# Kernel optimization log

Hardware: AMD Instinct MI355X
Metric: run time of the kernel (lower is better)

The kernel has to match this reference:

```python
import jax, jax.numpy as jnp
import numpy as np

D = 1024      # model_size
H = 16        # n_heads
HD = D // H   # head_size
B = 8
S = 1024


def setup_inputs() -> dict:
    key = jax.random.key(0)
    ks = jax.random.split(key, 8)
    sq = lambda k, shp: jax.random.normal(k, shp, dtype=jnp.float32) * (1.0 / np.sqrt(shp[0]))
    return {
        "query": jax.random.normal(ks[0], (B, S, D), dtype=jnp.float32),
        "value": jax.random.normal(ks[1], (B, S, D), dtype=jnp.float32),
        "Wq": sq(ks[2], (D, D)),
        "bq": jnp.zeros((D,), dtype=jnp.float32),
        "Wkv": sq(ks[3], (D, 2 * D)),
        "bkv": jnp.zeros((2 * D,), dtype=jnp.float32),
        "Wo": sq(ks[4], (D, D)),
        "bo": jnp.zeros((D,), dtype=jnp.float32),
    }


def reference(query, value, Wq, bq, Wkv, bkv, Wo, bo):
    scale = 1.0 / jnp.sqrt(jnp.float32(HD))
    q = query @ Wq + bq                      # [B,S,D]
    kv = value @ Wkv + bkv                   # [B,S,2D]
    # tf.split(kv, 2H): chunks 0..H-1 are K heads, H..2H-1 are V heads
    k = kv[..., :D].reshape(B, S, H, HD)
    v = kv[..., D:].reshape(B, S, H, HD)
    qh = q.reshape(B, S, H, HD)
    scores = jnp.einsum("bqhd,bkhd->bhqk", qh, k) * scale   # [B,H,S,S]
    attn = jax.nn.softmax(scores, axis=-1)
    heads = jnp.einsum("bhqk,bkhd->bqhd", attn, v).reshape(B, S, D)
    return heads @ Wo + bo
```

## Files before the change

### kernel.cpp

```cpp
#include <hip/hip_runtime.h>
#include <math.h>

#define B_  8
#define S_  1024
#define D_  1024
#define H_  16
#define HD_ 64

typedef float          floatx4  __attribute__((ext_vector_type(4)));
typedef __bf16         bf16x8   __attribute__((ext_vector_type(8)));
typedef unsigned short ushortx4 __attribute__((ext_vector_type(4)));
typedef unsigned int   uintx2   __attribute__((ext_vector_type(2)));
typedef unsigned int   uintx4   __attribute__((ext_vector_type(4)));

__device__ __forceinline__ unsigned short f2bf(float f) {
    union { float f; unsigned u; } v; v.f = f;
    unsigned r = v.u + 0x7FFFu + ((v.u >> 16) & 1u);
    return (unsigned short)(r >> 16);
}
__device__ __forceinline__ unsigned pk2(float a, float b) {
    union { __bf16 h[2]; unsigned u; } r;
    r.h[0] = (__bf16)a; r.h[1] = (__bf16)b;
    return r.u;
}
__device__ __forceinline__ void async16(const void* g, void* l) {
    __builtin_amdgcn_global_load_lds(
        (__attribute__((address_space(1))) void*)g,
        (__attribute__((address_space(3))) void*)l, 16, 0, 0);
}

__global__ __launch_bounds__(256) void cast2_k(const float* __restrict__ s0,
                                               const float* __restrict__ s1,
                                               unsigned short* __restrict__ d0,
                                               unsigned short* __restrict__ d1) {
    int i = blockIdx.x * 256 + threadIdx.x;
    floatx4 a = ((const floatx4*)s0)[i];
    floatx4 b = ((const floatx4*)s1)[i];
    ushortx4 oa = { f2bf(a[0]), f2bf(a[1]), f2bf(a[2]), f2bf(a[3]) };
    ushortx4 ob = { f2bf(b[0]), f2bf(b[1]), f2bf(b[2]), f2bf(b[3]) };
    ((ushortx4*)d0)[i] = oa;
    ((ushortx4*)d1)[i] = ob;
}

__global__ __launch_bounds__(256) void wtrans_all_k(const float* __restrict__ Wq,
                                                    const float* __restrict__ Wkv,
                                                    const float* __restrict__ Wo,
                                                    unsigned short* __restrict__ WqT,
                                                    unsigned short* __restrict__ WkvT,
                                                    unsigned short* __restrict__ WoT) {
    __shared__ float T[64 * 68];
    const int t = threadIdx.x;
    const int z = blockIdx.z;
    const float* W; unsigned short* WT; int Ndim, nbase;
    if (z == 0)      { W = Wq;  WT = WqT;  Ndim = 1024; nbase = 0; }
    else if (z == 3) { W = Wo;  WT = WoT;  Ndim = 1024; nbase = 0; }
    else             { W = Wkv; WT = WkvT; Ndim = 2048; nbase = (z - 1) * 1024; }
    const int n0 = blockIdx.x * 64 + nbase;
    const int k0 = blockIdx.y * 64;
#pragma unroll
    for (int rep = 0; rep < 4; ++rep) {
        int kl = (t >> 4) + rep * 16;
        int ns = (t & 15) * 4;
        *(floatx4*)(T + kl * 68 + ns) = *(const floatx4*)(W + (size_t)(k0 + kl) * Ndim + n0 + ns);
    }
    __syncthreads();
#pragma unroll
    for (int rep = 0; rep < 2; ++rep) {
        int nl = (t >> 3) + rep * 32;
        int ks = (t & 7) * 8;
        union { unsigned short s[8]; uintx4 u; } o;
#pragma unroll
        for (int j = 0; j < 8; ++j) o.s[j] = f2bf(T[(ks + j) * 68 + nl]);
        *(uintx4*)(WT + (size_t)(n0 + nl) * 1024 + k0 + ks) = o.u;
    }
}

__global__ __launch_bounds__(256) void vtrans_k(const unsigned short* __restrict__ KVb,
                                                unsigned short* __restrict__ Vtg) {
    __shared__ unsigned short T[64 * 72];
    const int t  = threadIdx.x;
    const int c0 = blockIdx.x * 64;
    const int s0 = blockIdx.y * 64;
    const int b  = blockIdx.z;
#pragma unroll
    for (int rep = 0; rep < 2; ++rep) {
        int sl = (t >> 3) + rep * 32;
        int cs = (t & 7) * 8;
        *(uintx4*)(T + sl * 72 + cs) =
            *(const uintx4*)(KVb + ((size_t)(b * 1024 + s0 + sl)) * 2048 + 1024 + c0 + cs);
    }
    __syncthreads();
#pragma unroll
    for (int rep = 0; rep < 2; ++rep) {
        int cl = (t >> 3) + rep * 32;
        int ss = (t & 7) * 8;
        union { unsigned short s[8]; uintx4 u; } o;
#pragma unroll
        for (int j = 0; j < 8; ++j) o.s[j] = T[(ss + j) * 72 + cl];
        *(uintx4*)(Vtg + ((size_t)(b * 1024 + c0 + cl)) * 1024 + s0 + ss) = o.u;
    }
}

template<int OUT_BF16>
__global__ __launch_bounds__(256) void gemm_bt(const unsigned short* __restrict__ A,
                                               const unsigned short* __restrict__ Bt,
                                               const float* __restrict__ bias,
                                               void* __restrict__ C,
                                               int M, int N, int K, float oscale) {
    __shared__ unsigned short As[128 * 32];
    __shared__ unsigned short Bs[128 * 32];
    const int t    = threadIdx.x;
    const int lane = t & 63;
    const int w    = t >> 6;
    const int quad = lane >> 4;
    const int l15  = lane & 15;
    const int m0   = blockIdx.x * 128;
    const int n0   = blockIdx.y * 128;
    const int wr   = (w >> 1) * 64;
    const int wc   = (w & 1) * 64;
    const int rowA = lane >> 2;
    const int kseg = (lane & 3) * 8;

    floatx4 acc[4][4] = {};

    const unsigned short* ga0 = A  + (size_t)(m0 + rowA) * K + kseg;
    const unsigned short* gb0 = Bt + (size_t)(n0 + rowA) * K + kseg;

    for (int k0 = 0; k0 < K; k0 += 32) {
#pragma unroll
        for (int i = 0; i < 2; ++i) {
            int c = i * 4 + w;
            async16(ga0 + (size_t)(c * 16) * K + k0, As + c * 512);
            async16(gb0 + (size_t)(c * 16) * K + k0, Bs + c * 512);
        }
        __syncthreads();
        bf16x8 af[4], bf[4];
#pragma unroll
        for (int mi = 0; mi < 4; ++mi)
            af[mi] = *(const bf16x8*)(As + (wr + mi * 16 + l15) * 32 + quad * 8);
#pragma unroll
        for (int ni = 0; ni < 4; ++ni)
            bf[ni] = *(const bf16x8*)(Bs + (wc + ni * 16 + l15) * 32 + quad * 8);
#pragma unroll
        for (int mi = 0; mi < 4; ++mi)
#pragma unroll
            for (int ni = 0; ni < 4; ++ni)
                acc[mi][ni] = __builtin_amdgcn_mfma_f32_16x16x32_bf16(af[mi], bf[ni], acc[mi][ni], 0, 0, 0);
        __syncthreads();
    }

#pragma unroll
    for (int ni = 0; ni < 4; ++ni) {
        const int col = n0 + wc + ni * 16 + l15;
        const float bv = bias[col];
#pragma unroll
        for (int mi = 0; mi < 4; ++mi) {
            const int row = m0 + wr + mi * 16 + quad * 4;
#pragma unroll
            for (int r = 0; r < 4; ++r) {
                float v = (acc[mi][ni][r] + bv) * oscale;
                if (OUT_BF16)
                    ((unsigned short*)C)[(size_t)(row + r) * N + col] = f2bf(v);
                else
                    ((float*)C)[(size_t)(row + r) * N + col] = v;
            }
        }
    }
}

__global__ __launch_bounds__(256) void attn_kernel(const unsigned short* __restrict__ Qb,
                                                   const unsigned short* __restrict__ KVb,
                                                   const unsigned short* __restrict__ Vtg,
                                                   unsigned short* __restrict__ Hb) {
    __shared__ unsigned short Qs[128 * 64];
    __shared__ unsigned short Ks[64 * 64];
    __shared__ unsigned short Vs[64 * 64];
    __shared__ unsigned short Ps[4 * 32 * 64];

    const int lin = blockIdx.x;
    const int xcd = lin & 7;
    const int grp = lin >> 3;
    const int bh  = xcd * 16 + (grp >> 3);
    const int qt  = grp & 7;
    const int b   = bh >> 4;
    const int h   = bh & 15;
    const int q0  = qt * 128;

    const int t    = threadIdx.x;
    const int lane = t & 63;
    const int w    = t >> 6;
    const int quad = lane >> 4;
    const int l15  = lane & 15;
    const int e7   = l15 & 7;
    const int lrow = lane >> 3;
    const int lswz = ((lane & 7) ^ lrow) * 8;

    {
        const unsigned short* gq = Qb + ((size_t)(b * S_ + q0)) * D_ + h * HD_;
#pragma unroll
        for (int i = 0; i < 4; ++i) {
            int r0 = (w * 4 + i) * 8;
            async16(gq + (size_t)(r0 + lrow) * D_ + lswz, Qs + r0 * 64);
        }
    }

    const unsigned short* gkbase = KVb + ((size_t)b * S_) * (2 * D_) + h * HD_;
    const unsigned short* gvbase = Vtg + ((size_t)(b * D_ + h * HD_)) * S_;

    float   lsum[2] = { 0.f, 0.f };
    floatx4 oacc[4][2] = {};
    unsigned short* Psw = Ps + w * (32 * 64);

    for (int k0 = 0; k0 < S_; k0 += 64) {
        __syncthreads();
#pragma unroll
        for (int j = 0; j < 2; ++j) {
            int r0 = (w * 2 + j) * 8;
            async16(gkbase + (size_t)(k0 + r0 + lrow) * (2 * D_) + lswz, Ks + r0 * 64);
            async16(gvbase + (size_t)(r0 + lrow) * S_ + k0 + lswz,      Vs + r0 * 64);
        }
        __syncthreads();

        floatx4 st[4][2] = {};
#pragma unroll
        for (int ks = 0; ks < 2; ++ks) {
            bf16x8 aK[4], bQ[2];
#pragma unroll
            for (int mi = 0; mi < 4; ++mi)
                aK[mi] = *(const bf16x8*)(Ks + (mi * 16 + l15) * 64 + ((ks * 4 + quad) ^ e7) * 8);
#pragma unroll
            for (int ni = 0; ni < 2; ++ni)
                bQ[ni] = *(const bf16x8*)(Qs + (w * 32 + ni * 16 + l15) * 64 + ((ks * 4 + quad) ^ e7) * 8);
#pragma unroll
            for (int mi = 0; mi < 4; ++mi)
#pragma unroll
                for (int ni = 0; ni < 2; ++ni)
                    st[mi][ni] = __builtin_amdgcn_mfma_f32_16x16x32_bf16(aK[mi], bQ[ni], st[mi][ni], 0, 0, 0);
        }

#pragma unroll
        for (int ni = 0; ni < 2; ++ni) {
            float ls = 0.f;
#pragma unroll
            for (int mi = 0; mi < 4; ++mi) {
                float p0 = __builtin_amdgcn_exp2f(st[mi][ni][0]);
                float p1 = __builtin_amdgcn_exp2f(st[mi][ni][1]);
                float p2 = __builtin_amdgcn_exp2f(st[mi][ni][2]);
                float p3 = __builtin_amdgcn_exp2f(st[mi][ni][3]);
                ls += (p0 + p1) + (p2 + p3);
                uintx2 pk = { pk2(p0, p1), pk2(p2, p3) };
                *(uintx2*)(Psw + (ni * 16 + l15) * 64 +
                           (((2 * mi + (quad >> 1)) ^ e7) * 8 + (quad & 1) * 4)) = pk;
            }
            lsum[ni] += ls;
        }

#pragma unroll
        for (int ks = 0; ks < 2; ++ks) {
            bf16x8 aV[4], bP[2];
#pragma unroll
            for (int mi = 0; mi < 4; ++mi)
                aV[mi] = *(const bf16x8*)(Vs + (mi * 16 + l15) * 64 + ((ks * 4 + quad) ^ e7) * 8);
#pragma unroll
            for (int ni = 0; ni < 2; ++ni)
                bP[ni] = *(const bf16x8*)(Psw + (ni * 16 + l15) * 64 + ((ks * 4 + quad) ^ e7) * 8);
#pragma unroll
            for (int mi = 0; mi < 4; ++mi)
#pragma unroll
                for (int ni = 0; ni < 2; ++ni)
                    oacc[mi][ni] = __builtin_amdgcn_mfma_f32_16x16x32_bf16(aV[mi], bP[ni], oacc[mi][ni], 0, 0, 0);
        }
    }

    float rl[2];
#pragma unroll
    for (int ni = 0; ni < 2; ++ni) {
        float l = lsum[ni];
        l += __shfl_xor(l, 16);
        l += __shfl_xor(l, 32);
        rl[ni] = 1.f / l;
    }
#pragma unroll
    for (int mi = 0; mi < 4; ++mi)
#pragma unroll
        for (int ni = 0; ni < 2; ++ni) {
            uintx2 pk = { pk2(oacc[mi][ni][0] * rl[ni], oacc[mi][ni][1] * rl[ni]),
                          pk2(oacc[mi][ni][2] * rl[ni], oacc[mi][ni][3] * rl[ni]) };
            *(uintx2*)(Psw + (ni * 16 + l15) * 64 +
                       (((2 * mi + (quad >> 1)) ^ e7) * 8 + (quad & 1) * 4)) = pk;
        }
    {
        int qrow = lane >> 1;
        int kh   = lane & 1;
        size_t obase = ((size_t)(b * S_ + q0 + w * 32 + qrow)) * D_ + h * HD_ + kh * 32;
        int e = qrow & 7;
#pragma unroll
        for (int j = 0; j < 4; ++j) {
            int chunk = kh * 4 + j;
            *(uintx4*)(Hb + obase + j * 8) =
                *(const uintx4*)(Psw + qrow * 64 + ((chunk ^ e) * 8));
        }
    }
}

extern "C" void kernel_launch(void* const* d_in, const int* in_sizes, int n_in,
                              void* d_out, int out_size, void* d_ws, size_t ws_size,
                              hipStream_t stream) {
    (void)in_sizes; (void)n_in; (void)out_size; (void)ws_size;
    const float* query = (const float*)d_in[0];
    const float* value = (const float*)d_in[1];
    const float* Wq    = (const float*)d_in[2];
    const float* bq    = (const float*)d_in[3];
    const float* Wkv   = (const float*)d_in[4];
    const float* bkv   = (const float*)d_in[5];
    const float* Wo    = (const float*)d_in[6];
    const float* bo    = (const float*)d_in[7];

    const size_t MS = (size_t)B_ * S_;
    char* p = (char*)d_ws;
    unsigned short* qbf  = (unsigned short*)p; p += MS * D_ * 2;
    unsigned short* vbf  = (unsigned short*)p; p += MS * D_ * 2;
    unsigned short* WqT  = (unsigned short*)p; p += (size_t)D_ * D_ * 2;
    unsigned short* WkvT = (unsigned short*)p; p += (size_t)2 * D_ * D_ * 2;
    unsigned short* WoT  = (unsigned short*)p; p += (size_t)D_ * D_ * 2;
    unsigned short* Qb   = (unsigned short*)p; p += MS * D_ * 2;
    unsigned short* KVb  = (unsigned short*)p; p += MS * 2 * D_ * 2;
    unsigned short* Hb   = (unsigned short*)p; p += MS * D_ * 2;
    unsigned short* Vtg  = qbf;

    const float cexp = 0.125f * 1.44269504088896341f;

    cast2_k<<<(int)(MS * D_ / 1024), 256, 0, stream>>>(query, value, qbf, vbf);
    wtrans_all_k<<<dim3(16, 16, 4), 256, 0, stream>>>(Wq, Wkv, Wo, WqT, WkvT, WoT);

    gemm_bt<1><<<dim3(64, 8),  256, 0, stream>>>(qbf, WqT,  bq,  Qb,  8192, 1024, 1024, cexp);
    gemm_bt<1><<<dim3(64, 16), 256, 0, stream>>>(vbf, WkvT, bkv, KVb, 8192, 2048, 1024, 1.0f);
    vtrans_k<<<dim3(16, 16, 8), 256, 0, stream>>>(KVb, Vtg);
    attn_kernel<<<1024, 256, 0, stream>>>(Qb, KVb, Vtg, Hb);
    gemm_bt<0><<<dim3(64, 8),  256, 0, stream>>>(Hb, WoT, bo, d_out, 8192, 1024, 1024, 1.0f);
}
```

Before: 313.2 us.

## Fuse prep kernels, write V transposed from KV GEMM, hoist Q fragments

Merges the input cast and weight transpose into one launch, and drops the separate V-transpose kernel by having the KV GEMM's V half write its output directly in transposed layout. The K output becomes a compact [M,1024] buffer. The GEMM epilogue swaps MFMA operand order so it can issue vectorized stores, and the attention kernel keeps Q fragments in registers so its Q shared buffer can be reused for P. Together these cut launch count and extra global round trips, at the cost of more register pressure and strided 8-byte stores for the transposed V.

```diff
diff --git a/kernel.cpp b/kernel.cpp
--- a/kernel.cpp
+++ b/kernel.cpp
@@ -29,34 +29,37 @@
         (__attribute__((address_space(3))) void*)l, 16, 0, 0);
 }
 
-__global__ __launch_bounds__(256) void cast2_k(const float* __restrict__ s0,
-                                               const float* __restrict__ s1,
-                                               unsigned short* __restrict__ d0,
-                                               unsigned short* __restrict__ d1) {
-    int i = blockIdx.x * 256 + threadIdx.x;
-    floatx4 a = ((const floatx4*)s0)[i];
-    floatx4 b = ((const floatx4*)s1)[i];
-    ushortx4 oa = { f2bf(a[0]), f2bf(a[1]), f2bf(a[2]), f2bf(a[3]) };
-    ushortx4 ob = { f2bf(b[0]), f2bf(b[1]), f2bf(b[2]), f2bf(b[3]) };
-    ((ushortx4*)d0)[i] = oa;
-    ((ushortx4*)d1)[i] = ob;
-}
-
-__global__ __launch_bounds__(256) void wtrans_all_k(const float* __restrict__ Wq,
-                                                    const float* __restrict__ Wkv,
-                                                    const float* __restrict__ Wo,
-                                                    unsigned short* __restrict__ WqT,
-                                                    unsigned short* __restrict__ WkvT,
-                                                    unsigned short* __restrict__ WoT) {
+__global__ __launch_bounds__(256) void prep_k(const float* __restrict__ query,
+                                              const float* __restrict__ value,
+                                              unsigned short* __restrict__ qbf,
+                                              unsigned short* __restrict__ vbf,
+                                              const float* __restrict__ Wq,
+                                              const float* __restrict__ Wkv,
+                                              const float* __restrict__ Wo,
+                                              unsigned short* __restrict__ WqT,
+                                              unsigned short* __restrict__ WkvT,
+                                              unsigned short* __restrict__ WoT) {
     __shared__ float T[64 * 68];
-    const int t = threadIdx.x;
-    const int z = blockIdx.z;
+    const int t   = threadIdx.x;
+    const int bid = blockIdx.x;
+    if (bid < 8192) {
+        int i = bid * 256 + t;
+        floatx4 a = ((const floatx4*)query)[i];
+        floatx4 b = ((const floatx4*)value)[i];
+        uintx2 oa = { pk2(a[0], a[1]), pk2(a[2], a[3]) };
+        uintx2 ob = { pk2(b[0], b[1]), pk2(b[2], b[3]) };
+        ((uintx2*)qbf)[i] = oa;
+        ((uintx2*)vbf)[i] = ob;
+        return;
+    }
+    const int lin = bid - 8192;
+    const int z   = lin >> 8;
     const float* W; unsigned short* WT; int Ndim, nbase;
     if (z == 0)      { W = Wq;  WT = WqT;  Ndim = 1024; nbase = 0; }
     else if (z == 3) { W = Wo;  WT = WoT;  Ndim = 1024; nbase = 0; }
     else             { W = Wkv; WT = WkvT; Ndim = 2048; nbase = (z - 1) * 1024; }
-    const int n0 = blockIdx.x * 64 + nbase;
-    const int k0 = blockIdx.y * 64;
+    const int n0 = (lin & 15) * 64 + nbase;
+    const int k0 = ((lin >> 4) & 15) * 64;
 #pragma unroll
     for (int rep = 0; rep < 4; ++rep) {
         int kl = (t >> 4) + rep * 16;
@@ -75,37 +78,12 @@
     }
 }
 
-__global__ __launch_bounds__(256) void vtrans_k(const unsigned short* __restrict__ KVb,
-                                                unsigned short* __restrict__ Vtg) {
-    __shared__ unsigned short T[64 * 72];
-    const int t  = threadIdx.x;
-    const int c0 = blockIdx.x * 64;
-    const int s0 = blockIdx.y * 64;
-    const int b  = blockIdx.z;
-#pragma unroll
-    for (int rep = 0; rep < 2; ++rep) {
-        int sl = (t >> 3) + rep * 32;
-        int cs = (t & 7) * 8;
-        *(uintx4*)(T + sl * 72 + cs) =
-            *(const uintx4*)(KVb + ((size_t)(b * 1024 + s0 + sl)) * 2048 + 1024 + c0 + cs);
-    }
-    __syncthreads();
-#pragma unroll
-    for (int rep = 0; rep < 2; ++rep) {
-        int cl = (t >> 3) + rep * 32;
-        int ss = (t & 7) * 8;
-        union { unsigned short s[8]; uintx4 u; } o;
-#pragma unroll
-        for (int j = 0; j < 8; ++j) o.s[j] = T[(ss + j) * 72 + cl];
-        *(uintx4*)(Vtg + ((size_t)(b * 1024 + c0 + cl)) * 1024 + s0 + ss) = o.u;
-    }
-}
-
-template<int OUT_BF16>
+template<int MODE>
 __global__ __launch_bounds__(256) void gemm_bt(const unsigned short* __restrict__ A,
                                                const unsigned short* __restrict__ Bt,
                                                const float* __restrict__ bias,
                                                void* __restrict__ C,
+                                               unsigned short* __restrict__ Vtg,
                                                int M, int N, int K, float oscale) {
     __shared__ unsigned short As[128 * 32];
     __shared__ unsigned short Bs[128 * 32];
@@ -120,6 +98,7 @@
     const int wc   = (w & 1) * 64;
     const int rowA = lane >> 2;
     const int kseg = (lane & 3) * 8;
+    const bool vmode = (MODE == 2) && (blockIdx.y >= 8);
 
     floatx4 acc[4][4] = {};
 
@@ -141,41 +120,71 @@
 #pragma unroll
         for (int ni = 0; ni < 4; ++ni)
             bf[ni] = *(const bf16x8*)(Bs + (wc + ni * 16 + l15) * 32 + quad * 8);
-#pragma unroll
-        for (int mi = 0; mi < 4; ++mi)
-#pragma unroll
-            for (int ni = 0; ni < 4; ++ni)
-                acc[mi][ni] = __builtin_amdgcn_mfma_f32_16x16x32_bf16(af[mi], bf[ni], acc[mi][ni], 0, 0, 0);
+        if (vmode) {
+#pragma unroll
+            for (int mi = 0; mi < 4; ++mi)
+#pragma unroll
+                for (int ni = 0; ni < 4; ++ni)
+                    acc[mi][ni] = __builtin_amdgcn_mfma_f32_16x16x32_bf16(af[mi], bf[ni], acc[mi][ni], 0, 0, 0);
+        } else {
+#pragma unroll
+            for (int mi = 0; mi < 4; ++mi)
+#pragma unroll
+                for (int ni = 0; ni < 4; ++ni)
+                    acc[mi][ni] = __builtin_amdgcn_mfma_f32_16x16x32_bf16(bf[ni], af[mi], acc[mi][ni], 0, 0, 0);
+        }
         __syncthreads();
     }
 
-#pragma unroll
-    for (int ni = 0; ni < 4; ++ni) {
-        const int col = n0 + wc + ni * 16 + l15;
-        const float bv = bias[col];
-#pragma unroll
-        for (int mi = 0; mi < 4; ++mi) {
-            const int row = m0 + wr + mi * 16 + quad * 4;
-#pragma unroll
-            for (int r = 0; r < 4; ++r) {
-                float v = (acc[mi][ni][r] + bv) * oscale;
-                if (OUT_BF16)
-                    ((unsigned short*)C)[(size_t)(row + r) * N + col] = f2bf(v);
-                else
-                    ((float*)C)[(size_t)(row + r) * N + col] = v;
+    if (MODE == 2 && vmode) {
+        const int bb = m0 >> 10;
+#pragma unroll
+        for (int ni = 0; ni < 4; ++ni) {
+            const int n = n0 + wc + ni * 16 + l15;
+            const int c = n - 1024;
+            const float bv = bias[n];
+#pragma unroll
+            for (int mi = 0; mi < 4; ++mi) {
+                const int m = m0 + wr + mi * 16 + quad * 4;
+                const int s = m & 1023;
+                floatx4 v = acc[mi][ni];
+                uintx2 o = { pk2(v[0] + bv, v[1] + bv), pk2(v[2] + bv, v[3] + bv) };
+                *(uintx2*)(Vtg + ((size_t)(bb * 1024 + c)) * 1024 + s) = o;
             }
         }
+    } else {
+        const int stride = (MODE == 2) ? 1024 : N;
+#pragma unroll
+        for (int ni = 0; ni < 4; ++ni) {
+            const int nb = n0 + wc + ni * 16 + quad * 4;
+            const floatx4 b4 = *(const floatx4*)(bias + nb);
+#pragma unroll
+            for (int mi = 0; mi < 4; ++mi) {
+                const int m = m0 + wr + mi * 16 + l15;
+                floatx4 v = acc[mi][ni];
+                float v0 = (v[0] + b4[0]) * oscale;
+                float v1 = (v[1] + b4[1]) * oscale;
+                float v2 = (v[2] + b4[2]) * oscale;
+                float v3 = (v[3] + b4[3]) * oscale;
+                if (MODE == 1) {
+                    floatx4 o = { v0, v1, v2, v3 };
+                    *(floatx4*)((float*)C + (size_t)m * stride + nb) = o;
+                } else {
+                    uintx2 o = { pk2(v0, v1), pk2(v2, v3) };
+                    *(uintx2*)((unsigned short*)C + (size_t)m * stride + nb) = o;
+                }
+            }
+        }
     }
 }
 
 __global__ __launch_bounds__(256) void attn_kernel(const unsigned short* __restrict__ Qb,
-                                                   const unsigned short* __restrict__ KVb,
+                                                   const unsigned short* __restrict__ Kb,
                                                    const unsigned short* __restrict__ Vtg,
                                                    unsigned short* __restrict__ Hb) {
-    __shared__ unsigned short Qs[128 * 64];
+    __shared__ unsigned short QPs[128 * 64];
     __shared__ unsigned short Ks[64 * 64];
     __shared__ unsigned short Vs[64 * 64];
-    __shared__ unsigned short Ps[4 * 32 * 64];
 
     const int lin = blockIdx.x;
     const int xcd = lin & 7;
@@ -200,42 +209,47 @@
 #pragma unroll
         for (int i = 0; i < 4; ++i) {
             int r0 = (w * 4 + i) * 8;
-            async16(gq + (size_t)(r0 + lrow) * D_ + lswz, Qs + r0 * 64);
-        }
-    }
-
-    const unsigned short* gkbase = KVb + ((size_t)b * S_) * (2 * D_) + h * HD_;
+            async16(gq + (size_t)(r0 + lrow) * D_ + lswz, QPs + r0 * 64);
+        }
+    }
+    __syncthreads();
+
+    bf16x8 bQ[2][2];
+#pragma unroll
+    for (int ks = 0; ks < 2; ++ks)
+#pragma unroll
+        for (int ni = 0; ni < 2; ++ni)
+            bQ[ks][ni] = *(const bf16x8*)(QPs + (w * 32 + ni * 16 + l15) * 64 + ((ks * 4 + quad) ^ e7) * 8);
+
+    const unsigned short* gkbase = Kb  + ((size_t)b * S_) * D_ + h * HD_;
     const unsigned short* gvbase = Vtg + ((size_t)(b * D_ + h * HD_)) * S_;
 
     float   lsum[2] = { 0.f, 0.f };
     floatx4 oacc[4][2] = {};
-    unsigned short* Psw = Ps + w * (32 * 64);
+    unsigned short* Psw = QPs + w * (32 * 64);
 
     for (int k0 = 0; k0 < S_; k0 += 64) {
         __syncthreads();
 #pragma unroll
         for (int j = 0; j < 2; ++j) {
             int r0 = (w * 2 + j) * 8;
-            async16(gkbase + (size_t)(k0 + r0 + lrow) * (2 * D_) + lswz, Ks + r0 * 64);
-            async16(gvbase + (size_t)(r0 + lrow) * S_ + k0 + lswz,      Vs + r0 * 64);
+            async16(gkbase + (size_t)(k0 + r0 + lrow) * D_ + lswz, Ks + r0 * 64);
+            async16(gvbase + (size_t)(r0 + lrow) * S_ + k0 + lswz, Vs + r0 * 64);
         }
         __syncthreads();
 
         floatx4 st[4][2] = {};
 #pragma unroll
         for (int ks = 0; ks < 2; ++ks) {
-            bf16x8 aK[4], bQ[2];
+            bf16x8 aK[4];
 #pragma unroll
             for (int mi = 0; mi < 4; ++mi)
                 aK[mi] = *(const bf16x8*)(Ks + (mi * 16 + l15) * 64 + ((ks * 4 + quad) ^ e7) * 8);
 #pragma unroll
-            for (int ni = 0; ni < 2; ++ni)
-                bQ[ni] = *(const bf16x8*)(Qs + (w * 32 + ni * 16 + l15) * 64 + ((ks * 4 + quad) ^ e7) * 8);
-#pragma unroll
             for (int mi = 0; mi < 4; ++mi)
 #pragma unroll
                 for (int ni = 0; ni < 2; ++ni)
-                    st[mi][ni] = __builtin_amdgcn_mfma_f32_16x16x32_bf16(aK[mi], bQ[ni], st[mi][ni], 0, 0, 0);
+                    st[mi][ni] = __builtin_amdgcn_mfma_f32_16x16x32_bf16(aK[mi], bQ[ks][ni], st[mi][ni], 0, 0, 0);
         }
 
 #pragma unroll
@@ -324,18 +338,15 @@
     unsigned short* WkvT = (unsigned short*)p; p += (size_t)2 * D_ * D_ * 2;
     unsigned short* WoT  = (unsigned short*)p; p += (size_t)D_ * D_ * 2;
     unsigned short* Qb   = (unsigned short*)p; p += MS * D_ * 2;
-    unsigned short* KVb  = (unsigned short*)p; p += MS * 2 * D_ * 2;
+    unsigned short* Kb   = (unsigned short*)p; p += MS * D_ * 2;
     unsigned short* Hb   = (unsigned short*)p; p += MS * D_ * 2;
     unsigned short* Vtg  = qbf;
 
     const float cexp = 0.125f * 1.44269504088896341f;
 
-    cast2_k<<<(int)(MS * D_ / 1024), 256, 0, stream>>>(query, value, qbf, vbf);
-    wtrans_all_k<<<dim3(16, 16, 4), 256, 0, stream>>>(Wq, Wkv, Wo, WqT, WkvT, WoT);
-
-    gemm_bt<1><<<dim3(64, 8),  256, 0, stream>>>(qbf, WqT,  bq,  Qb,  8192, 1024, 1024, cexp);
-    gemm_bt<1><<<dim3(64, 16), 256, 0, stream>>>(vbf, WkvT, bkv, KVb, 8192, 2048, 1024, 1.0f);
-    vtrans_k<<<dim3(16, 16, 8), 256, 0, stream>>>(KVb, Vtg);
-    attn_kernel<<<1024, 256, 0, stream>>>(Qb, KVb, Vtg, Hb);
-    gemm_bt<0><<<dim3(64, 8),  256, 0, stream>>>(Hb, WoT, bo, d_out, 8192, 1024, 1024, 1.0f);
-}
+    prep_k<<<9216, 256, 0, stream>>>(query, value, qbf, vbf, Wq, Wkv, Wo, WqT, WkvT, WoT);
+    gemm_bt<0><<<dim3(64, 8),  256, 0, stream>>>(qbf, WqT,  bq,  Qb, nullptr, 8192, 1024, 1024, cexp);
+    gemm_bt<2><<<dim3(64, 16), 256, 0, stream>>>(vbf, WkvT, bkv, Kb, Vtg,     8192, 2048, 1024, 1.0f);
+    attn_kernel<<<1024, 256, 0, stream>>>(Qb, Kb, Vtg, Hb);
+    gemm_bt<1><<<dim3(64, 8),  256, 0, stream>>>(Hb, WoT, bo, d_out, nullptr, 8192, 1024, 1024, 1.0f);
+}
```

Result: slower. 322.5 us (+3.0%).
